# Performance work log

Hardware: AMD Instinct MI355X
Metric: run time of the kernel (lower is better)

Reference implementation:

```python
import jax, jax.numpy as jnp
import numpy as np

C = 512
NUM_HEADS = 8
NUM_GROUPS = 32
EPS = 1e-6


def group_norm(x, gamma, beta):
    # x: [B, C, N]
    b, c, n = x.shape
    xg = x.reshape(b, NUM_GROUPS, (c // NUM_GROUPS) * n)
    mean = xg.mean(axis=-1, keepdims=True)
    var = xg.var(axis=-1, keepdims=True)
    xg = (xg - mean) * jax.lax.rsqrt(var + EPS)
    x = xg.reshape(b, c, n)
    return x * gamma[None, :, None] + beta[None, :, None]


def conv1x1(x, w, bias):
    # pointwise conv: w [out_c, in_c], x [B, C, N]
    return jnp.einsum('oc,bcn->bon', w, x) + bias[None, :, None]


def setup_inputs() -> dict:
    key = jax.random.key(0)
    ks = jax.random.split(key, 11)
    s = 1.0 / np.sqrt(C)
    inp = {
        'x': jax.random.normal(ks[0], (4, C, 2048), dtype=jnp.float32),
        'gn_gamma': jnp.ones((C,), jnp.float32),
        'gn_beta': jnp.zeros((C,), jnp.float32),
        'q_w': jax.random.uniform(ks[1], (C, C), jnp.float32, -s, s),
        'q_b': jax.random.uniform(ks[2], (C,), jnp.float32, -s, s),
        'k_w': jax.random.uniform(ks[3], (C, C), jnp.float32, -s, s),
        'k_b': jax.random.uniform(ks[4], (C,), jnp.float32, -s, s),
        'v_w': jax.random.uniform(ks[5], (C, C), jnp.float32, -s, s),
        'v_b': jax.random.uniform(ks[6], (C,), jnp.float32, -s, s),
        'proj_w': jax.random.uniform(ks[7], (C, C), jnp.float32, -s, s),
        'proj_b': jax.random.uniform(ks[8], (C,), jnp.float32, -s, s),
    }
    return inp


def reference(x, gn_gamma, gn_beta, q_w, q_b, k_w, k_b, v_w, v_b, proj_w, proj_b):
    b, c, n = x.shape
    hc = c // NUM_HEADS
    h_ = group_norm(x, gn_gamma, gn_beta)
    q = conv1x1(h_, q_w, q_b)
    k = conv1x1(h_, k_w, k_b)
    v = conv1x1(h_, v_w, v_b)
    # split heads: [B, H, hc, N]
    q = q.reshape(b, NUM_HEADS, hc, n)
    k = k.reshape(b, NUM_HEADS, hc, n)
    v = v.reshape(b, NUM_HEADS, hc, n)
    # NOTE: scale uses full channel count c, matching the original code
    scale = jnp.asarray(c, x.dtype) ** -0.5
    # scores: [B, H, Nq, Nk]
    w = jnp.einsum('bhcn,bhcm->bhnm', q, k) * scale
    w = jax.nn.softmax(w, axis=-1)
    # out[b,h,c,q] = sum_m v[b,h,c,m] * w[b,h,q,m]
    out = jnp.einsum('bhcm,bhqm->bhcq', v, w)
    out = out.reshape(b, c, n)
    out = conv1x1(out, proj_w, proj_b)
    return x + out
```

## Files before the change

kernel.cpp:

```cpp
#include <hip/hip_runtime.h>
#include <hip/hip_bf16.h>
#include <math.h>

#define C_DIM 512
#define N_DIM 2048
#define B_DIM 4
#define NGRP 32
#define GCH 16
#define NHEAD 8
#define HDIM 64
#define EPSV 1e-6f

using f32x4  = __attribute__((ext_vector_type(4))) float;
using bf16x8 = __attribute__((ext_vector_type(8))) short;

#define GLL16(gp, lp) __builtin_amdgcn_global_load_lds( \
    (const __attribute__((address_space(1))) unsigned int*)(gp), \
    (__attribute__((address_space(3))) unsigned int*)(lp), 16, 0, 0)

#define BFPACK(a, b) __builtin_amdgcn_perm(__float_as_uint(b), __float_as_uint(a), 0x07060302u)

static __device__ __forceinline__ unsigned short f2bf(float f) {
    union { __hip_bfloat16 h; unsigned short u; } cv;
    cv.h = __float2bfloat16(f);
    return cv.u;
}

__global__ __launch_bounds__(256) void gn_stats(const float* __restrict__ x,
                                                float* __restrict__ stats) {
    const int GSZ = GCH * N_DIM;
    int bg = blockIdx.x;
    const float4* x4 = (const float4*)(x + (size_t)bg * GSZ);
    int tid = threadIdx.x;

    float s = 0.f, ss = 0.f;
    #pragma unroll
    for (int it = 0; it < GSZ / 4 / 256; ++it) {
        float4 v = x4[tid + it * 256];
        s  += v.x + v.y + v.z + v.w;
        ss += v.x * v.x + v.y * v.y + v.z * v.z + v.w * v.w;
    }
    __shared__ float rs[256], rss[256];
    rs[tid] = s; rss[tid] = ss;
    __syncthreads();
    for (int off = 128; off > 0; off >>= 1) {
        if (tid < off) { rs[tid] += rs[tid + off]; rss[tid] += rss[tid + off]; }
        __syncthreads();
    }
    if (tid == 0) {
        float mean = rs[0] * (1.f / GSZ);
        float var  = rss[0] * (1.f / GSZ) - mean * mean;
        stats[bg * 2]     = mean;
        stats[bg * 2 + 1] = rsqrtf(var + EPSV);
    }
}

__global__ __launch_bounds__(256) void gn_apply_t(const float* __restrict__ x,
                                                  const float* __restrict__ stats,
                                                  const float* __restrict__ gamma,
                                                  const float* __restrict__ beta,
                                                  unsigned short* __restrict__ ht) {
    __shared__ char smem[8192];
    int n0 = blockIdx.x * 64, c0 = blockIdx.y * 64, b = blockIdx.z;
    int tid = threadIdx.x;
    #pragma unroll
    for (int it = 0; it < 4; ++it) {
        int idx = tid + it * 256;
        int ci = idx >> 4, n4 = (idx & 15) << 2;
        int cg = c0 + ci, grp = cg >> 4;
        float mean = stats[(b * NGRP + grp) * 2];
        float rstd = stats[(b * NGRP + grp) * 2 + 1];
        float ga = gamma[cg] * rstd, be = beta[cg] - mean * ga;
        float4 v = *(const float4*)&x[((size_t)b * C_DIM + cg) * N_DIM + n0 + n4];
        float vals[4] = {v.x, v.y, v.z, v.w};
        #pragma unroll
        for (int j = 0; j < 4; ++j) {
            int nl = n4 + j;
            *(unsigned short*)(smem + nl * 128 + ((ci * 2) ^ ((nl & 7) << 4))) =
                f2bf(vals[j] * ga + be);
        }
    }
    __syncthreads();
    #pragma unroll
    for (int i = 0; i < 2; ++i) {
        int idx = tid + i * 256;
        int row = idx >> 3, ch = idx & 7;
        bf16x8 v = *(const bf16x8*)(smem + row * 128 + ((ch * 16) ^ ((row & 7) << 4)));
        *(bf16x8*)&ht[((size_t)(b * N_DIM + n0 + row)) * C_DIM + c0 + ch * 8] = v;
    }
}

__global__ __launch_bounds__(256) void cast4_bf16(const float* __restrict__ s0,
                                                  const float* __restrict__ s1,
                                                  const float* __restrict__ s2,
                                                  const float* __restrict__ s3,
                                                  unsigned short* __restrict__ dst) {
    int which = blockIdx.y;
    const float* src = (which == 0) ? s0 : (which == 1) ? s1 : (which == 2) ? s2 : s3;
    size_t idx = (size_t)blockIdx.x * 256 + threadIdx.x;
    const float4* s4 = (const float4*)src;
    float4 a = s4[idx * 2], b = s4[idx * 2 + 1];
    bf16x8 o;
    o[0] = (short)f2bf(a.x); o[1] = (short)f2bf(a.y);
    o[2] = (short)f2bf(a.z); o[3] = (short)f2bf(a.w);
    o[4] = (short)f2bf(b.x); o[5] = (short)f2bf(b.y);
    o[6] = (short)f2bf(b.z); o[7] = (short)f2bf(b.w);
    *(bf16x8*)&dst[(size_t)which * 262144 + idx * 8] = o;
}

__global__ __launch_bounds__(256) void conv_qkv(const unsigned short* __restrict__ Wall,
                                                const float* __restrict__ q_b,
                                                const float* __restrict__ k_b,
                                                const float* __restrict__ v_b,
                                                const unsigned short* __restrict__ ht,
                                                unsigned short* __restrict__ qt,
                                                unsigned short* __restrict__ kt,
                                                unsigned short* __restrict__ vt,
                                                float escale) {
    __shared__ char smem[32768];

    int bn0 = blockIdx.x * 64;
    int bo  = blockIdx.y * 64;
    int tid = threadIdx.x;
    int L = tid & 63, w = tid >> 6;
    int g = L >> 4, c = L & 15;
    int wr = w >> 1, wc = w & 1;

    f32x4 acc[3][2][2];
    #pragma unroll
    for (int w3 = 0; w3 < 3; ++w3)
        #pragma unroll
        for (int t = 0; t < 2; ++t)
            #pragma unroll
            for (int u = 0; u < 2; ++u) acc[w3][t][u] = f32x4{0.f, 0.f, 0.f, 0.f};

    const unsigned short* sbase;
    char* ldsb;
    if (w == 0) { sbase = ht + (size_t)bn0 * C_DIM; ldsb = smem; }
    else { sbase = Wall + (size_t)(w - 1) * 262144 + (size_t)bo * C_DIM; ldsb = smem + w * 8192; }

    for (int k0 = 0; k0 < C_DIM; k0 += 64) {
        #pragma unroll
        for (int i = 0; i < 8; ++i) {
            int row = i * 8 + (L >> 3);
            int sl = (L & 7) ^ (row & 7);
            GLL16(sbase + (size_t)row * C_DIM + k0 + sl * 8, ldsb + i * 1024);
        }
        __syncthreads();

        bf16x8 bfr[2][2];
        #pragma unroll
        for (int u = 0; u < 2; ++u) {
            int row = wc * 32 + u * 16 + c;
            #pragma unroll
            for (int ks = 0; ks < 2; ++ks)
                bfr[u][ks] = *(const bf16x8*)(smem + row * 128 +
                                              ((g * 16 + ks * 64) ^ ((row & 7) << 4)));
        }
        #pragma unroll
        for (int w3 = 0; w3 < 3; ++w3) {
            char* As = smem + 8192 + w3 * 8192;
            bf16x8 af[2][2];
            #pragma unroll
            for (int t = 0; t < 2; ++t) {
                int row = wr * 32 + t * 16 + c;
                #pragma unroll
                for (int ks = 0; ks < 2; ++ks)
                    af[t][ks] = *(const bf16x8*)(As + row * 128 +
                                                 ((g * 16 + ks * 64) ^ ((row & 7) << 4)));
            }
            #pragma unroll
            for (int ks = 0; ks < 2; ++ks)
                #pragma unroll
                for (int t = 0; t < 2; ++t)
                    #pragma unroll
                    for (int u = 0; u < 2; ++u)
                        acc[w3][t][u] = __builtin_amdgcn_mfma_f32_16x16x32_bf16(
                            af[t][ks], bfr[u][ks], acc[w3][t][u], 0, 0, 0);
        }
        __syncthreads();
    }

    int b  = bn0 >> 11;
    int nb = bn0 & (N_DIM - 1);
    int hh = bo >> 6;
    int bh = b * NHEAD + hh;

    #pragma unroll
    for (int t = 0; t < 2; ++t)
        #pragma unroll
        for (int r = 0; r < 4; ++r) {
            int m = bo + wr * 32 + t * 16 + g * 4 + r;
            float bi = v_b[m];
            #pragma unroll
            for (int u = 0; u < 2; ++u) {
                int n = nb + wc * 32 + u * 16 + c;
                vt[((size_t)b * C_DIM + m) * N_DIM + n] = f2bf(acc[2][t][u][r] + bi);
            }
        }

    char* Ts = smem;
    #pragma unroll
    for (int pass = 0; pass < 2; ++pass) {
        const float* bias = pass ? k_b : q_b;
        float esc = pass ? 1.0f : escale;
        unsigned short* dst = pass ? kt : qt;
        __syncthreads();
        #pragma unroll
        for (int t = 0; t < 2; ++t)
            #pragma unroll
            for (int r = 0; r < 4; ++r) {
                int ml = wr * 32 + t * 16 + g * 4 + r;
                float bi = bias[bo + ml];
                #pragma unroll
                for (int u = 0; u < 2; ++u) {
                    int nl = wc * 32 + u * 16 + c;
                    *(unsigned short*)(Ts + nl * 128 + ((ml * 2) ^ ((nl & 7) << 4))) =
                        f2bf((acc[pass][t][u][r] + bi) * esc);
                }
            }
        __syncthreads();
        #pragma unroll
        for (int i = 0; i < 2; ++i) {
            int idx = tid + i * 256;
            int row = idx >> 3, ch = idx & 7;
            bf16x8 v = *(const bf16x8*)(Ts + row * 128 + ((ch * 16) ^ ((row & 7) << 4)));
            *(bf16x8*)&dst[((size_t)bh * N_DIM + nb + row) * HDIM + ch * 8] = v;
        }
    }
}

__global__ __launch_bounds__(256) void conv_proj(const unsigned short* __restrict__ Wb,
                                                 const float* __restrict__ bias,
                                                 const unsigned short* __restrict__ Bsrc,
                                                 const float* __restrict__ res,
                                                 float* __restrict__ outf) {
    __shared__ char smem[24576];
    int bn0 = blockIdx.x * 128;
    int bo  = blockIdx.y * 64;
    int tid = threadIdx.x;
    int L = tid & 63, w = tid >> 6;
    int g = L >> 4, c = L & 15;
    int wr = w >> 1, wc = w & 1;

    f32x4 acc[2][4];
    #pragma unroll
    for (int t = 0; t < 2; ++t)
        #pragma unroll
        for (int u = 0; u < 4; ++u) acc[t][u] = f32x4{0.f, 0.f, 0.f, 0.f};

    for (int k0 = 0; k0 < C_DIM; k0 += 64) {
        #pragma unroll
        for (int i = 0; i < 2; ++i) {
            int j = w * 2 + i;
            int ra = j * 8 + (L >> 3);
            int sl = (L & 7) ^ (ra & 7);
            GLL16(Wb + (size_t)(bo + ra) * C_DIM + k0 + sl * 8, smem + j * 1024);
        }
        #pragma unroll
        for (int i = 0; i < 4; ++i) {
            int j = w * 4 + i;
            int rb = j * 8 + (L >> 3);
            int sl = (L & 7) ^ (rb & 7);
            GLL16(Bsrc + (size_t)(bn0 + rb) * C_DIM + k0 + sl * 8, smem + 8192 + j * 1024);
        }
        __syncthreads();

        bf16x8 af[2][2], bfr[4][2];
        #pragma unroll
        for (int t = 0; t < 2; ++t) {
            int row = wr * 32 + t * 16 + c;
            #pragma unroll
            for (int ks = 0; ks < 2; ++ks)
                af[t][ks] = *(const bf16x8*)(smem + row * 128 +
                                             ((g * 16 + ks * 64) ^ ((row & 7) << 4)));
        }
        #pragma unroll
        for (int u = 0; u < 4; ++u) {
            int row = wc * 64 + u * 16 + c;
            #pragma unroll
            for (int ks = 0; ks < 2; ++ks)
                bfr[u][ks] = *(const bf16x8*)(smem + 8192 + row * 128 +
                                              ((g * 16 + ks * 64) ^ ((row & 7) << 4)));
        }
        #pragma unroll
        for (int ks = 0; ks < 2; ++ks)
            #pragma unroll
            for (int t = 0; t < 2; ++t)
                #pragma unroll
                for (int u = 0; u < 4; ++u)
                    acc[t][u] = __builtin_amdgcn_mfma_f32_16x16x32_bf16(
                        af[t][ks], bfr[u][ks], acc[t][u], 0, 0, 0);
        __syncthreads();
    }

    int b  = bn0 >> 11;
    int nb = bn0 & (N_DIM - 1);
    #pragma unroll
    for (int t = 0; t < 2; ++t)
        #pragma unroll
        for (int r = 0; r < 4; ++r) {
            int m = bo + wr * 32 + t * 16 + g * 4 + r;
            float bi = bias[m];
            #pragma unroll
            for (int u = 0; u < 4; ++u) {
                int n = nb + wc * 64 + u * 16 + c;
                size_t off = ((size_t)b * C_DIM + m) * N_DIM + n;
                outf[off] = acc[t][u][r] + bi + res[off];
            }
        }
}

__global__ __launch_bounds__(512, 4) void attn_kernel(const unsigned short* __restrict__ Qt,
                                                      const unsigned short* __restrict__ Kt,
                                                      const unsigned short* __restrict__ Vt,
                                                      unsigned short* __restrict__ at) {
    __shared__ char smem[49152];

    int q0 = blockIdx.x * 128;
    int bh = blockIdx.y;
    int b = bh >> 3, hh = bh & 7;
    int tid = threadIdx.x;
    int L = tid & 63, w = tid >> 6;
    int g = L >> 4, c = L & 15;

    const unsigned short* Qh = Qt + (size_t)bh * N_DIM * HDIM;
    const unsigned short* Kh = Kt + (size_t)bh * N_DIM * HDIM;
    const unsigned short* Vh = Vt + (size_t)bh * HDIM * N_DIM;

    #pragma unroll
    for (int i = 0; i < 2; ++i) {
        int j = w * 2 + i;
        int row = j * 8 + (L >> 3);
        int sl = (L & 7) ^ (row & 7);
        GLL16(Qh + (size_t)(q0 + row) * HDIM + sl * 8, smem + j * 1024);
    }
    int srow = w * 8 + (L >> 3);
    int ssl  = (L & 7) ^ (srow & 7);
    GLL16(Kh + (size_t)srow * HDIM + ssl * 8, smem + 16384 + w * 1024);
    GLL16(Vh + (size_t)srow * N_DIM + ssl * 8, smem + 24576 + w * 1024);
    __syncthreads();

    int csw = (c & 7) << 4;
    char* kb0 = smem + 16384 + c * 128 + ((g * 16) ^ csw);
    char* kb1 = smem + 16384 + c * 128 + ((g * 16 + 64) ^ csw);
    char* pb  = smem + (w * 16 + c) * 128;
    char* pw0 = pb + ((g * 8) ^ csw);
    char* pw1 = pb + ((32 + g * 8) ^ csw);
    char* pw2 = pb + ((64 + g * 8) ^ csw);
    char* pw3 = pb + ((96 + g * 8) ^ csw);
    char* pr0 = pb + ((g * 16) ^ csw);
    char* pr1 = pb + ((64 + g * 16) ^ csw);

    bf16x8 qf[2];
    qf[0] = *(const bf16x8*)pr0;
    qf[1] = *(const bf16x8*)pr1;

    const unsigned short* kgp = Kh + (size_t)(64 + srow) * HDIM + ssl * 8;
    const unsigned short* vgp = Vh + (size_t)srow * N_DIM + 64 + ssl * 8;

    f32x4 oacc[4];
    #pragma unroll
    for (int t = 0; t < 4; ++t) oacc[t] = f32x4{0.f, 0.f, 0.f, 0.f};
    float m_r = -INFINITY, l_part = 0.f;

    auto tile = [&](int BOFF) {
        f32x4 sacc[4];
        #pragma unroll
        for (int t = 0; t < 4; ++t) sacc[t] = f32x4{0.f, 0.f, 0.f, 0.f};
        __builtin_amdgcn_s_setprio(1);
        #pragma unroll
        for (int t = 0; t < 4; ++t) {
            bf16x8 kf0 = *(const bf16x8*)(kb0 + BOFF + t * 2048);
            bf16x8 kf1 = *(const bf16x8*)(kb1 + BOFF + t * 2048);
            sacc[t] = __builtin_amdgcn_mfma_f32_16x16x32_bf16(kf0, qf[0], sacc[t], 0, 0, 0);
            sacc[t] = __builtin_amdgcn_mfma_f32_16x16x32_bf16(kf1, qf[1], sacc[t], 0, 0, 0);
        }
        __builtin_amdgcn_s_setprio(0);

        float t0 = fmaxf(fmaxf(sacc[0][0], sacc[0][1]), sacc[0][2]);
        float t1 = fmaxf(fmaxf(sacc[0][3], sacc[1][0]), sacc[1][1]);
        float t2 = fmaxf(fmaxf(sacc[1][2], sacc[1][3]), sacc[2][0]);
        float t3 = fmaxf(fmaxf(sacc[2][1], sacc[2][2]), sacc[2][3]);
        float t4 = fmaxf(fmaxf(sacc[3][0], sacc[3][1]), sacc[3][2]);
        float mloc = fmaxf(fmaxf(fmaxf(t0, t1), fmaxf(t2, t3)), fmaxf(t4, sacc[3][3]));
        if (!__all(mloc - m_r <= 6.0f)) {
            mloc = fmaxf(mloc, __shfl_xor(mloc, 16));
            mloc = fmaxf(mloc, __shfl_xor(mloc, 32));
            float mn = fmaxf(m_r, mloc);
            float fac = exp2f(m_r - mn);
            m_r = mn;
            l_part *= fac;
            #pragma unroll
            for (int t = 0; t < 4; ++t) oacc[t] = oacc[t] * fac;
        }
        float rs = 0.f;
        unsigned pk[4][2];
        #pragma unroll
        for (int t = 0; t < 4; ++t) {
            float p0 = exp2f(sacc[t][0] - m_r);
            float p1 = exp2f(sacc[t][1] - m_r);
            float p2 = exp2f(sacc[t][2] - m_r);
            float p3 = exp2f(sacc[t][3] - m_r);
            rs += (p0 + p1) + (p2 + p3);
            pk[t][0] = BFPACK(p0, p1);
            pk[t][1] = BFPACK(p2, p3);
        }
        l_part += rs;

        *(unsigned long long*)pw0 = (unsigned long long)pk[0][0] | ((unsigned long long)pk[0][1] << 32);
        *(unsigned long long*)pw1 = (unsigned long long)pk[1][0] | ((unsigned long long)pk[1][1] << 32);
        *(unsigned long long*)pw2 = (unsigned long long)pk[2][0] | ((unsigned long long)pk[2][1] << 32);
        *(unsigned long long*)pw3 = (unsigned long long)pk[3][0] | ((unsigned long long)pk[3][1] << 32);

        __builtin_amdgcn_s_setprio(1);
        {
            bf16x8 pf0 = *(const bf16x8*)pr0;
            #pragma unroll
            for (int t = 0; t < 4; ++t) {
                bf16x8 vf = *(const bf16x8*)(kb0 + BOFF + 8192 + t * 2048);
                oacc[t] = __builtin_amdgcn_mfma_f32_16x16x32_bf16(vf, pf0, oacc[t], 0, 0, 0);
            }
            bf16x8 pf1 = *(const bf16x8*)pr1;
            #pragma unroll
            for (int t = 0; t < 4; ++t) {
                bf16x8 vf = *(const bf16x8*)(kb1 + BOFF + 8192 + t * 2048);
                oacc[t] = __builtin_amdgcn_mfma_f32_16x16x32_bf16(vf, pf1, oacc[t], 0, 0, 0);
            }
        }
        __builtin_amdgcn_s_setprio(0);
    };

    for (int i = 0; i < 16; ++i) {
        GLL16(kgp, smem + 32768 + w * 1024);
        GLL16(vgp, smem + 40960 + w * 1024);
        kgp += 64 * HDIM;
        vgp += 64;
        tile(0);
        __syncthreads();
        if (i < 15) {
            GLL16(kgp, smem + 16384 + w * 1024);
            GLL16(vgp, smem + 24576 + w * 1024);
            kgp += 64 * HDIM;
            vgp += 64;
        }
        tile(16384);
        __syncthreads();
    }

    float l_r = l_part;
    l_r += __shfl_xor(l_r, 16);
    l_r += __shfl_xor(l_r, 32);
    float oinv = 1.f / l_r;
    {
        unsigned lo, hi;
        lo = BFPACK(oacc[0][0] * oinv, oacc[0][1] * oinv);
        hi = BFPACK(oacc[0][2] * oinv, oacc[0][3] * oinv);
        *(unsigned long long*)pw0 = (unsigned long long)lo | ((unsigned long long)hi << 32);
        lo = BFPACK(oacc[1][0] * oinv, oacc[1][1] * oinv);
        hi = BFPACK(oacc[1][2] * oinv, oacc[1][3] * oinv);
        *(unsigned long long*)pw1 = (unsigned long long)lo | ((unsigned long long)hi << 32);
        lo = BFPACK(oacc[2][0] * oinv, oacc[2][1] * oinv);
        hi = BFPACK(oacc[2][2] * oinv, oacc[2][3] * oinv);
        *(unsigned long long*)pw2 = (unsigned long long)lo | ((unsigned long long)hi << 32);
        lo = BFPACK(oacc[3][0] * oinv, oacc[3][1] * oinv);
        hi = BFPACK(oacc[3][2] * oinv, oacc[3][3] * oinv);
        *(unsigned long long*)pw3 = (unsigned long long)lo | ((unsigned long long)hi << 32);
    }
    char* wbase = smem + w * 2048;
    #pragma unroll
    for (int i = 0; i < 2; ++i) {
        int idx = L + i * 64;
        int row = idx >> 3, ch = idx & 7;
        bf16x8 v = *(const bf16x8*)(wbase + row * 128 + ((ch * 16) ^ ((row & 7) << 4)));
        *(bf16x8*)&at[((size_t)(b * N_DIM + q0 + w * 16 + row)) * C_DIM + hh * HDIM + ch * 8] = v;
    }
}

extern "C" void kernel_launch(void* const* d_in, const int* in_sizes, int n_in,
                              void* d_out, int out_size, void* d_ws, size_t ws_size,
                              hipStream_t stream) {
    (void)in_sizes; (void)n_in; (void)out_size; (void)ws_size;
    const float* x     = (const float*)d_in[0];
    const float* gam   = (const float*)d_in[1];
    const float* bet   = (const float*)d_in[2];
    const float* q_w   = (const float*)d_in[3];
    const float* q_b   = (const float*)d_in[4];
    const float* k_w   = (const float*)d_in[5];
    const float* k_b   = (const float*)d_in[6];
    const float* v_w   = (const float*)d_in[7];
    const float* v_b   = (const float*)d_in[8];
    const float* p_w   = (const float*)d_in[9];
    const float* p_b   = (const float*)d_in[10];
    float* out = (float*)d_out;

    const size_t MB = 1 << 20;
    char* wsb = (char*)d_ws;
    unsigned short* ht  = (unsigned short*)(wsb);
    unsigned short* wqb = (unsigned short*)(wsb + 8 * MB);
    unsigned short* wpb = (unsigned short*)(wsb + 9 * MB + 512 * 1024);
    float*          stats = (float*)(wsb + 10 * MB);
    unsigned short* qt  = (unsigned short*)(wsb + 11 * MB);
    unsigned short* kt  = (unsigned short*)(wsb + 19 * MB);
    unsigned short* vt  = (unsigned short*)(wsb + 27 * MB);
    unsigned short* at  = (unsigned short*)(wsb + 35 * MB);

    gn_stats<<<B_DIM * NGRP, 256, 0, stream>>>(x, stats);
    gn_apply_t<<<dim3(N_DIM / 64, C_DIM / 64, B_DIM), 256, 0, stream>>>(x, stats, gam, bet, ht);

    cast4_bf16<<<dim3(128, 4), 256, 0, stream>>>(q_w, k_w, v_w, p_w, wqb);

    const float escale = 0.044194173824159216f * 1.4426950408889634f;
    conv_qkv<<<dim3(B_DIM * N_DIM / 64, C_DIM / 64), 256, 0, stream>>>(
        wqb, q_b, k_b, v_b, ht, qt, kt, vt, escale);

    attn_kernel<<<dim3(N_DIM / 128, B_DIM * NHEAD), 512, 0, stream>>>(qt, kt, vt, at);

    conv_proj<<<dim3(B_DIM * N_DIM / 128, C_DIM / 64), 256, 0, stream>>>(wpb, p_b, at, x, out);
}
```

Before: 116.5 us.

## Split GN stats across two blocks, widen QKV conv tile, vectorize softmax exp

Group-norm statistics are now computed by two blocks per group, each writing partial sums, and the apply kernel combines them and computes mean and rstd inline. This doubles the parallelism of the stats pass. The QKV pointwise conv moves to 512-thread blocks covering 128 tokens, so each weight tile loaded into LDS is reused across twice as many tokens, at the cost of more LDS per block. The attention softmax exp step is restructured into vector form with a vector row-sum reduction.

```diff
diff --git a/kernel.cpp b/kernel.cpp
--- a/kernel.cpp
+++ b/kernel.cpp
@@ -27,15 +27,15 @@
 }
 
 __global__ __launch_bounds__(256) void gn_stats(const float* __restrict__ x,
-                                                float* __restrict__ stats) {
-    const int GSZ = GCH * N_DIM;
-    int bg = blockIdx.x;
-    const float4* x4 = (const float4*)(x + (size_t)bg * GSZ);
+                                                float* __restrict__ partial) {
+    const int HSZ = GCH * N_DIM / 2;
+    int blk = blockIdx.x;
+    const float4* x4 = (const float4*)(x + (size_t)blk * HSZ);
     int tid = threadIdx.x;
 
     float s = 0.f, ss = 0.f;
     #pragma unroll
-    for (int it = 0; it < GSZ / 4 / 256; ++it) {
+    for (int it = 0; it < HSZ / 4 / 256; ++it) {
         float4 v = x4[tid + it * 256];
         s  += v.x + v.y + v.z + v.w;
         ss += v.x * v.x + v.y * v.y + v.z * v.z + v.w * v.w;
@@ -48,19 +48,18 @@
         __syncthreads();
     }
     if (tid == 0) {
-        float mean = rs[0] * (1.f / GSZ);
-        float var  = rss[0] * (1.f / GSZ) - mean * mean;
-        stats[bg * 2]     = mean;
-        stats[bg * 2 + 1] = rsqrtf(var + EPSV);
+        partial[blk * 2]     = rs[0];
+        partial[blk * 2 + 1] = rss[0];
     }
 }
 
 __global__ __launch_bounds__(256) void gn_apply_t(const float* __restrict__ x,
-                                                  const float* __restrict__ stats,
+                                                  const float* __restrict__ partial,
                                                   const float* __restrict__ gamma,
                                                   const float* __restrict__ beta,
                                                   unsigned short* __restrict__ ht) {
     __shared__ char smem[8192];
+    const float GSZI = 1.f / (GCH * N_DIM);
     int n0 = blockIdx.x * 64, c0 = blockIdx.y * 64, b = blockIdx.z;
     int tid = threadIdx.x;
     #pragma unroll
@@ -68,8 +67,12 @@
         int idx = tid + it * 256;
         int ci = idx >> 4, n4 = (idx & 15) << 2;
         int cg = c0 + ci, grp = cg >> 4;
-        float mean = stats[(b * NGRP + grp) * 2];
-        float rstd = stats[(b * NGRP + grp) * 2 + 1];
+        int bg = b * NGRP + grp;
+        float s  = partial[bg * 4]     + partial[bg * 4 + 2];
+        float ss = partial[bg * 4 + 1] + partial[bg * 4 + 3];
+        float mean = s * GSZI;
+        float var  = ss * GSZI - mean * mean;
+        float rstd = rsqrtf(var + EPSV);
         float ga = gamma[cg] * rstd, be = beta[cg] - mean * ga;
         float4 v = *(const float4*)&x[((size_t)b * C_DIM + cg) * N_DIM + n0 + n4];
         float vals[4] = {v.x, v.y, v.z, v.w};
@@ -108,7 +111,7 @@
     *(bf16x8*)&dst[(size_t)which * 262144 + idx * 8] = o;
 }
 
-__global__ __launch_bounds__(256) void conv_qkv(const unsigned short* __restrict__ Wall,
+__global__ __launch_bounds__(512) void conv_qkv(const unsigned short* __restrict__ Wall,
                                                 const float* __restrict__ q_b,
                                                 const float* __restrict__ k_b,
                                                 const float* __restrict__ v_b,
@@ -117,14 +120,14 @@
                                                 unsigned short* __restrict__ kt,
                                                 unsigned short* __restrict__ vt,
                                                 float escale) {
-    __shared__ char smem[32768];
-
-    int bn0 = blockIdx.x * 64;
+    __shared__ char smem[40960];
+
+    int bn0 = blockIdx.x * 128;
     int bo  = blockIdx.y * 64;
     int tid = threadIdx.x;
     int L = tid & 63, w = tid >> 6;
     int g = L >> 4, c = L & 15;
-    int wr = w >> 1, wc = w & 1;
+    int wr = w >> 2, wc = w & 3;
 
     f32x4 acc[3][2][2];
     #pragma unroll
@@ -134,17 +137,25 @@
             #pragma unroll
             for (int u = 0; u < 2; ++u) acc[w3][t][u] = f32x4{0.f, 0.f, 0.f, 0.f};
 
-    const unsigned short* sbase;
-    char* ldsb;
-    if (w == 0) { sbase = ht + (size_t)bn0 * C_DIM; ldsb = smem; }
-    else { sbase = Wall + (size_t)(w - 1) * 262144 + (size_t)bo * C_DIM; ldsb = smem + w * 8192; }
-
     for (int k0 = 0; k0 < C_DIM; k0 += 64) {
-        #pragma unroll
-        for (int i = 0; i < 8; ++i) {
-            int row = i * 8 + (L >> 3);
-            int sl = (L & 7) ^ (row & 7);
-            GLL16(sbase + (size_t)row * C_DIM + k0 + sl * 8, ldsb + i * 1024);
+        if (w < 4) {
+            #pragma unroll
+            for (int i = 0; i < 4; ++i) {
+                int j = w * 4 + i;
+                int row = j * 8 + (L >> 3);
+                int sl = (L & 7) ^ (row & 7);
+                GLL16(ht + (size_t)(bn0 + row) * C_DIM + k0 + sl * 8, smem + j * 1024);
+            }
+        } else {
+            #pragma unroll
+            for (int i = 0; i < 6; ++i) {
+                int j = (w - 4) * 6 + i;
+                int w3 = j >> 3, jj = j & 7;
+                int row = jj * 8 + (L >> 3);
+                int sl = (L & 7) ^ (row & 7);
+                GLL16(Wall + (size_t)w3 * 262144 + (size_t)(bo + row) * C_DIM + k0 + sl * 8,
+                      smem + 16384 + j * 1024);
+            }
         }
         __syncthreads();
 
@@ -159,7 +170,7 @@
         }
         #pragma unroll
         for (int w3 = 0; w3 < 3; ++w3) {
-            char* As = smem + 8192 + w3 * 8192;
+            char* As = smem + 16384 + w3 * 8192;
             bf16x8 af[2][2];
             #pragma unroll
             for (int t = 0; t < 2; ++t) {
@@ -222,7 +233,7 @@
         __syncthreads();
         #pragma unroll
         for (int i = 0; i < 2; ++i) {
-            int idx = tid + i * 256;
+            int idx = tid + i * 512;
             int row = idx >> 3, ch = idx & 7;
             bf16x8 v = *(const bf16x8*)(Ts + row * 128 + ((ch * 16) ^ ((row & 7) << 4)));
             *(bf16x8*)&dst[((size_t)bh * N_DIM + nb + row) * HDIM + ch * 8] = v;
@@ -394,19 +405,25 @@
             #pragma unroll
             for (int t = 0; t < 4; ++t) oacc[t] = oacc[t] * fac;
         }
-        float rs = 0.f;
+        f32x4 m4 = {m_r, m_r, m_r, m_r};
+        f32x4 p[4];
+        #pragma unroll
+        for (int t = 0; t < 4; ++t) {
+            f32x4 d = sacc[t] - m4;
+            p[t][0] = exp2f(d[0]);
+            p[t][1] = exp2f(d[1]);
+            p[t][2] = exp2f(d[2]);
+            p[t][3] = exp2f(d[3]);
+        }
+        f32x4 racc = (p[0] + p[1]) + (p[2] + p[3]);
+        l_part += (racc[0] + racc[1]) + (racc[2] + racc[3]);
+
         unsigned pk[4][2];
         #pragma unroll
         for (int t = 0; t < 4; ++t) {
-            float p0 = exp2f(sacc[t][0] - m_r);
-            float p1 = exp2f(sacc[t][1] - m_r);
-            float p2 = exp2f(sacc[t][2] - m_r);
-            float p3 = exp2f(sacc[t][3] - m_r);
-            rs += (p0 + p1) + (p2 + p3);
-            pk[t][0] = BFPACK(p0, p1);
-            pk[t][1] = BFPACK(p2, p3);
-        }
-        l_part += rs;
+            pk[t][0] = BFPACK(p[t][0], p[t][1]);
+            pk[t][1] = BFPACK(p[t][2], p[t][3]);
+        }
 
         *(unsigned long long*)pw0 = (unsigned long long)pk[0][0] | ((unsigned long long)pk[0][1] << 32);
         *(unsigned long long*)pw1 = (unsigned long long)pk[1][0] | ((unsigned long long)pk[1][1] << 32);
@@ -499,19 +516,19 @@
     unsigned short* ht  = (unsigned short*)(wsb);
     unsigned short* wqb = (unsigned short*)(wsb + 8 * MB);
     unsigned short* wpb = (unsigned short*)(wsb + 9 * MB + 512 * 1024);
-    float*          stats = (float*)(wsb + 10 * MB);
+    float*          partial = (float*)(wsb + 10 * MB);
     unsigned short* qt  = (unsigned short*)(wsb + 11 * MB);
     unsigned short* kt  = (unsigned short*)(wsb + 19 * MB);
     unsigned short* vt  = (unsigned short*)(wsb + 27 * MB);
     unsigned short* at  = (unsigned short*)(wsb + 35 * MB);
 
-    gn_stats<<<B_DIM * NGRP, 256, 0, stream>>>(x, stats);
-    gn_apply_t<<<dim3(N_DIM / 64, C_DIM / 64, B_DIM), 256, 0, stream>>>(x, stats, gam, bet, ht);
+    gn_stats<<<B_DIM * NGRP * 2, 256, 0, stream>>>(x, partial);
+    gn_apply_t<<<dim3(N_DIM / 64, C_DIM / 64, B_DIM), 256, 0, stream>>>(x, partial, gam, bet, ht);
 
     cast4_bf16<<<dim3(128, 4), 256, 0, stream>>>(q_w, k_w, v_w, p_w, wqb);
 
     const float escale = 0.044194173824159216f * 1.4426950408889634f;
-    conv_qkv<<<dim3(B_DIM * N_DIM / 64, C_DIM / 64), 256, 0, stream>>>(
+    conv_qkv<<<dim3(B_DIM * N_DIM / 128, C_DIM / 64), 512, 0, stream>>>(
         wqb, q_b, k_b, v_b, ht, qt, kt, vt, escale);
 
     attn_kernel<<<dim3(N_DIM / 128, B_DIM * NHEAD), 512, 0, stream>>>(qt, kt, vt, at);
```

Result: no change. 115.9 us (-0.5%).
